# Optimization experiments

Measured on AMD Instinct MI355X. Metric: run time of the kernel, lower is better.

## Reference

```python
import jax, jax.numpy as jnp
import numpy as np

NUM_SHAPES, NUM_COLORS, NUM_CLASSES = 8, 8, 10
HID = 64
N_NODES, N_EDGES, N_REL, N_GRAPHS = 100000, 1600000, 3, 1024


def setup_inputs() -> dict:
    key = jax.random.key(0)
    ks = jax.random.split(key, 16)
    f = jnp.float32
    inp = {
        "x_idx": jax.random.randint(ks[0], (N_NODES, 2), 0, NUM_SHAPES),
        "edge_index": jax.random.randint(ks[1], (2, N_EDGES), 0, N_NODES),
        "edge_type": jax.random.randint(ks[2], (N_EDGES,), 0, N_REL),
        "batch": jnp.sort(jax.random.randint(ks[3], (N_NODES,), 0, N_GRAPHS)),
        # parameters (Linear weights stored as [in, out])
        "shape_emb": jax.random.normal(ks[4], (NUM_SHAPES, 8), f),
        "color_emb": jax.random.normal(ks[5], (NUM_COLORS, 8), f),
        "lin0_w": jax.random.normal(ks[6], (16, HID), f) * 0.1,
        "lin0_b": jnp.zeros((HID,), f),
        "r1_wrel": jax.random.normal(ks[7], (N_REL, HID, HID), f) * 0.05,
        "r1_wroot": jax.random.normal(ks[8], (HID, HID), f) * 0.05,
        "r1_b": jnp.zeros((HID,), f),
        "r2_wrel": jax.random.normal(ks[9], (N_REL, HID, HID), f) * 0.05,
        "r2_wroot": jax.random.normal(ks[10], (HID, HID), f) * 0.05,
        "r2_b": jnp.zeros((HID,), f),
        "cls_w": jax.random.normal(ks[11], (HID, NUM_CLASSES), f) * 0.1,
        "cls_b": jnp.zeros((NUM_CLASSES,), f),
    }
    return inp


def _rgcn(x, edge_index, edge_type, w_rel, w_root, b):
    # PyG RGCNConv with aggr='mean': per-relation mean of transformed neighbors + root + bias
    n = x.shape[0]
    xw = jnp.einsum('nd,rde->rne', x, w_rel)            # [R, N, H] (cheap dense)
    src, dst = edge_index[0], edge_index[1]
    msg = xw[edge_type, src]                            # [E, H] gather
    seg = edge_type * n + dst                           # combined (relation, node) segment id
    sums = jax.ops.segment_sum(msg, seg, num_segments=N_REL * n)
    cnt = jax.ops.segment_sum(jnp.ones_like(seg, dtype=x.dtype), seg, num_segments=N_REL * n)
    mean = sums / jnp.maximum(cnt, 1.0)[:, None]
    agg = mean.reshape(N_REL, n, -1).sum(axis=0)        # sum over relations
    return agg + x @ w_root + b


def reference(x_idx, edge_index, edge_type, batch,
              shape_emb, color_emb, lin0_w, lin0_b,
              r1_wrel, r1_wroot, r1_b, r2_wrel, r2_wroot, r2_b,
              cls_w, cls_b):
    x = jnp.concatenate([shape_emb[x_idx[:, 0]], color_emb[x_idx[:, 1]]], axis=1)  # [N, 16]
    x = jax.nn.relu(x @ lin0_w + lin0_b)
    x = jax.nn.relu(_rgcn(x, edge_index, edge_type, r1_wrel, r1_wroot, r1_b))
    x = jax.nn.relu(_rgcn(x, edge_index, edge_type, r2_wrel, r2_wroot, r2_b))
    # global mean pool over graphs
    sums = jax.ops.segment_sum(x, batch, num_segments=N_GRAPHS)
    cnt = jax.ops.segment_sum(jnp.ones((x.shape[0],), x.dtype), batch, num_segments=N_GRAPHS)
    pooled = sums / jnp.maximum(cnt, 1.0)[:, None]
    return pooled @ cls_w + cls_b
```

## Files before the change

### kernel.cpp

```cpp
#include <hip/hip_runtime.h>

#define NN 100000
#define NE 1600000
#define NRL 3
#define NG 1024
#define NBUCK 782
#define NXCD 8
#define PSTRIDE 384
#define BSLOTS (NXCD * PSTRIDE)
#define NKEY 384
#define OSTRIDE 392

typedef __attribute__((ext_vector_type(8))) short bf16x8;
typedef __attribute__((ext_vector_type(4))) float f32x4;

__device__ __forceinline__ int xcd_id() {
    unsigned int x;
    asm volatile("s_getreg_b32 %0, hwreg(HW_REG_XCC_ID)" : "=s"(x));
    return (int)(x & 7);
}

__device__ __forceinline__ unsigned short f2bf(float f) {
    unsigned u = __float_as_uint(f);
    unsigned r = (u + 0x7fffu + ((u >> 16) & 1u)) >> 16;
    return (unsigned short)r;
}

__global__ void k_embed(const int* __restrict__ x_idx,
                        const float* __restrict__ semb, const float* __restrict__ cemb,
                        const float* __restrict__ w, const float* __restrict__ b,
                        float* __restrict__ xout, unsigned short* __restrict__ xbf) {
    __shared__ float s_w[16 * 64];
    __shared__ float s_se[64], s_ce[64], s_b[64];
    int t = threadIdx.x;
    for (int i = t; i < 16 * 64; i += 256) s_w[i] = w[i];
    if (t < 64) { s_se[t] = semb[t]; s_ce[t] = cemb[t]; s_b[t] = b[t]; }
    __syncthreads();
    int gid = blockIdx.x * 256 + t;
    int v = gid >> 6, h = gid & 63;
    int si = x_idx[2 * v], ci = x_idx[2 * v + 1];
    float acc = s_b[h];
#pragma unroll
    for (int d = 0; d < 8; ++d) acc += s_se[si * 8 + d] * s_w[d * 64 + h];
#pragma unroll
    for (int d = 0; d < 8; ++d) acc += s_ce[ci * 8 + d] * s_w[(8 + d) * 64 + h];
    float r = fmaxf(acc, 0.f);
    xout[gid] = r;
    xbf[gid] = f2bf(r);
}

__global__ void k_bucket(const int* __restrict__ ei, const int* __restrict__ et,
                         int* __restrict__ bcnt, unsigned int* __restrict__ arena) {
    int e = blockIdx.x * 256 + threadIdx.x;
    if (e >= NE) return;
    int p = xcd_id();
    int src = __builtin_nontemporal_load(ei + e);
    int dst = __builtin_nontemporal_load(ei + NE + e);
    int rel = __builtin_nontemporal_load(et + e);
    int b = dst >> 7;
    unsigned int rec = (unsigned int)src | ((unsigned int)rel << 17) |
                       ((unsigned int)(dst & 127) << 19);
    int cell = b * NXCD + p;
    int pos = atomicAdd(&bcnt[cell], 1);
    if (pos < PSTRIDE) arena[(size_t)cell * PSTRIDE + pos] = rec;
}

__global__ __launch_bounds__(256) void k_sortbucket(
        const int* __restrict__ bcnt, unsigned int* __restrict__ arena,
        unsigned short* __restrict__ off16) {
    __shared__ unsigned int s_rec[BSLOTS];
    __shared__ unsigned int s_srt[BSLOTS];
    __shared__ int s_hist[NKEY + 1], s_start[NKEY + 1], s_pos[NKEY];
    int t = threadIdx.x;
    int b = blockIdx.x;

    for (int i = t; i < NKEY + 1; i += 256) s_hist[i] = 0;
    __syncthreads();

    int tot = 0;
#pragma unroll
    for (int p = 0; p < NXCD; ++p) {
        int c = bcnt[b * NXCD + p]; if (c > PSTRIDE) c = PSTRIDE;
        const unsigned int* src = arena + ((size_t)(b * NXCD + p)) * PSTRIDE;
        for (int i = t; i < c; i += 256) {
            unsigned int r = __builtin_nontemporal_load(src + i);
            s_rec[tot + i] = r;
            int key = ((r >> 19) & 127) * 3 + ((r >> 17) & 3);
            atomicAdd(&s_hist[key], 1);
        }
        tot += c;
    }
    __syncthreads();
    if (t == 0) {
        int run = 0;
#pragma unroll 8
        for (int k = 0; k < NKEY; ++k) { s_start[k] = run; run += s_hist[k]; }
        s_start[NKEY] = run;
    }
    __syncthreads();
    for (int i = t; i < NKEY; i += 256) s_pos[i] = s_start[i];
    __syncthreads();
    for (int i = t; i < tot; i += 256) {
        unsigned int r = s_rec[i];
        int key = ((r >> 19) & 127) * 3 + ((r >> 17) & 3);
        int p = atomicAdd(&s_pos[key], 1);
        s_srt[p] = r & 0x1FFFF;
    }
    __syncthreads();
    for (int i = t; i < tot; i += 256)
        arena[(size_t)b * BSLOTS + i] = s_srt[i];
    for (int i = t; i < NKEY + 1; i += 256)
        off16[(size_t)b * OSTRIDE + i] = (unsigned short)s_start[i];
}

__global__ void k_agg(const unsigned short* __restrict__ xbf,
                      const unsigned int* __restrict__ arena,
                      const unsigned short* __restrict__ off16,
                      unsigned short* __restrict__ K) {
    int wid = (blockIdx.x * 256 + threadIdx.x) >> 6;
    int lane = threadIdx.x & 63;
    if (wid >= NN) return;
    int v = wid;
    int b = v >> 7, dlo = v & 127;
    const unsigned short* ofs = off16 + (size_t)b * OSTRIDE + dlo * 3;
    int s0 = __builtin_amdgcn_readfirstlane((int)ofs[0]);
    int s1 = __builtin_amdgcn_readfirstlane((int)ofs[1]);
    int s2 = __builtin_amdgcn_readfirstlane((int)ofs[2]);
    int s3 = __builtin_amdgcn_readfirstlane((int)ofs[3]);
    const unsigned int* base = arena + (size_t)b * BSLOTS;

    int half = lane >> 5, sl = lane & 31;
    float2 a0 = {0.f, 0.f}, a1 = {0.f, 0.f}, a2 = {0.f, 0.f};

    int e = s0;
    for (; e + 8 <= s3; e += 8) {
#pragma unroll
        for (int k = 0; k < 4; ++k) {
            int ee = e + 2 * k + half;
            int idx = (int)base[ee];
            unsigned u = *reinterpret_cast<const unsigned*>(
                             xbf + (size_t)idx * 64 + 2 * sl);
            float f0 = __uint_as_float(u << 16);
            float f1 = __uint_as_float(u & 0xFFFF0000u);
            bool c0 = ee < s1;
            bool c2 = ee >= s2;
            bool c1 = !c0 && !c2;
            a0.x += c0 ? f0 : 0.f;  a0.y += c0 ? f1 : 0.f;
            a1.x += c1 ? f0 : 0.f;  a1.y += c1 ? f1 : 0.f;
            a2.x += c2 ? f0 : 0.f;  a2.y += c2 ? f1 : 0.f;
        }
    }
    for (; e < s3; e += 2) {
        int ee = e + half;
        bool ok = ee < s3;
        int idx = (int)base[ok ? ee : e];
        unsigned u = *reinterpret_cast<const unsigned*>(
                         xbf + (size_t)idx * 64 + 2 * sl);
        float f0 = __uint_as_float(u << 16);
        float f1 = __uint_as_float(u & 0xFFFF0000u);
        bool c0 = ok && (ee < s1);
        bool c2 = ok && (ee >= s2);
        bool c1 = ok && !(ee < s1) && (ee < s2);
        a0.x += c0 ? f0 : 0.f;  a0.y += c0 ? f1 : 0.f;
        a1.x += c1 ? f0 : 0.f;  a1.y += c1 ? f1 : 0.f;
        a2.x += c2 ? f0 : 0.f;  a2.y += c2 ? f1 : 0.f;
    }

    a0.x += __shfl_xor(a0.x, 32);  a0.y += __shfl_xor(a0.y, 32);
    a1.x += __shfl_xor(a1.x, 32);  a1.y += __shfl_xor(a1.y, 32);
    a2.x += __shfl_xor(a2.x, 32);  a2.y += __shfl_xor(a2.y, 32);

    unsigned short* Kv = K + (size_t)v * 256;
    if (lane < 32) {
        float d0 = fmaxf((float)(s1 - s0), 1.f);
        float d1 = fmaxf((float)(s2 - s1), 1.f);
        float d2 = fmaxf((float)(s3 - s2), 1.f);
        unsigned p0 = (unsigned)f2bf(a0.x / d0) | ((unsigned)f2bf(a0.y / d0) << 16);
        unsigned p1 = (unsigned)f2bf(a1.x / d1) | ((unsigned)f2bf(a1.y / d1) << 16);
        unsigned p2 = (unsigned)f2bf(a2.x / d2) | ((unsigned)f2bf(a2.y / d2) << 16);
        unsigned* Kw = reinterpret_cast<unsigned*>(Kv);
        Kw[sl]      = p0;
        Kw[32 + sl] = p1;
        Kw[64 + sl] = p2;
    }
    Kv[192 + lane] = xbf[(size_t)v * 64 + lane];
}

__global__ __launch_bounds__(512, 4) void k_transform(
        const unsigned short* __restrict__ K, const float* __restrict__ wrel,
        const float* __restrict__ wroot, const float* __restrict__ b,
        float* __restrict__ xout, unsigned short* __restrict__ xbf) {
    __shared__ __align__(16) unsigned short s_bf[4][8][64][8];
    __shared__ float s_b[64];
    int t = threadIdx.x;
    for (int i = t; i < 4 * 8 * 64 * 8; i += 512) {
        int j  = i & 7;
        int l  = (i >> 3) & 63;
        int c  = (i >> 9) & 7;
        int nt = (i >> 12) & 3;
        int k  = c * 32 + (l >> 4) * 8 + j;
        int n  = nt * 16 + (l & 15);
        const float* src = (k < 192) ? (wrel + k * 64 + n) : (wroot + (k - 192) * 64 + n);
        s_bf[nt][c][l][j] = f2bf(*src);
    }
    if (t < 64) s_b[t] = b[t];
    __syncthreads();

    int wave = t >> 6, lane = t & 63;
    int strip = blockIdx.x * 8 + wave;
    if (strip > NN / 16 - 1) strip = NN / 16 - 1;
    int v0 = strip * 16;

    const unsigned short* Ka = K + (size_t)(v0 + (lane & 15)) * 256 + (lane >> 4) * 8;

    f32x4 acc0 = {0.f, 0.f, 0.f, 0.f};
    f32x4 acc1 = {0.f, 0.f, 0.f, 0.f};
    f32x4 acc2 = {0.f, 0.f, 0.f, 0.f};
    f32x4 acc3 = {0.f, 0.f, 0.f, 0.f};

#pragma unroll
    for (int c = 0; c < 8; ++c) {
        bf16x8 a = *reinterpret_cast<const bf16x8*>(Ka + c * 32);
        bf16x8 b0 = *reinterpret_cast<const bf16x8*>(&s_bf[0][c][lane][0]);
        bf16x8 b1 = *reinterpret_cast<const bf16x8*>(&s_bf[1][c][lane][0]);
        bf16x8 b2 = *reinterpret_cast<const bf16x8*>(&s_bf[2][c][lane][0]);
        bf16x8 b3 = *reinterpret_cast<const bf16x8*>(&s_bf[3][c][lane][0]);
        acc0 = __builtin_amdgcn_mfma_f32_16x16x32_bf16(a, b0, acc0, 0, 0, 0);
        acc1 = __builtin_amdgcn_mfma_f32_16x16x32_bf16(a, b1, acc1, 0, 0, 0);
        acc2 = __builtin_amdgcn_mfma_f32_16x16x32_bf16(a, b2, acc2, 0, 0, 0);
        acc3 = __builtin_amdgcn_mfma_f32_16x16x32_bf16(a, b3, acc3, 0, 0, 0);
    }

    int col = lane & 15, rg = (lane >> 4) * 4;
#pragma unroll
    for (int r = 0; r < 4; ++r) {
        float o0 = fmaxf(acc0[r] + s_b[0  + col], 0.f);
        float o1 = fmaxf(acc1[r] + s_b[16 + col], 0.f);
        float o2 = fmaxf(acc2[r] + s_b[32 + col], 0.f);
        float o3 = fmaxf(acc3[r] + s_b[48 + col], 0.f);
        float* op = xout + (size_t)(v0 + rg + r) * 64;
        op[0  + col] = o0;
        op[16 + col] = o1;
        op[32 + col] = o2;
        op[48 + col] = o3;
        if (xbf) {
            unsigned short* ob = xbf + (size_t)(v0 + rg + r) * 64;
            ob[0  + col] = f2bf(o0);
            ob[16 + col] = f2bf(o1);
            ob[32 + col] = f2bf(o2);
            ob[48 + col] = f2bf(o3);
        }
    }
}

#define POOL_CHUNK 32
__global__ void k_pool(const float* __restrict__ x, const int* __restrict__ batch,
                       float* __restrict__ psum, int* __restrict__ pcnt) {
    int gwid = (blockIdx.x * 256 + threadIdx.x) >> 6;
    int lane = threadIdx.x & 63;
    int v0 = gwid * POOL_CHUNK;
    if (v0 >= NN) return;
    int v1 = v0 + POOL_CHUNK; if (v1 > NN) v1 = NN;
    float acc = 0.f;
    int cnt = 0;
    int gcur = batch[v0];
    for (int v = v0; v < v1; ++v) {
        int g = batch[v];
        if (g != gcur) {
            atomicAdd(&psum[gcur * 64 + lane], acc);
            if (lane == 0) atomicAdd(&pcnt[gcur], cnt);
            acc = 0.f; cnt = 0; gcur = g;
        }
        acc += x[(size_t)v * 64 + lane];
        ++cnt;
    }
    atomicAdd(&psum[gcur * 64 + lane], acc);
    if (lane == 0) atomicAdd(&pcnt[gcur], cnt);
}

__global__ void k_cls(const float* __restrict__ psum, const int* __restrict__ pcnt,
                      const float* __restrict__ w, const float* __restrict__ b,
                      float* __restrict__ out) {
    int gid = blockIdx.x * 256 + threadIdx.x;
    if (gid >= NG * 10) return;
    int g = gid / 10, c = gid % 10;
    float inv = 1.f / fmaxf((float)pcnt[g], 1.f);
    float acc = 0.f;
#pragma unroll
    for (int d = 0; d < 64; ++d) acc += psum[g * 64 + d] * w[d * 10 + c];
    out[gid] = acc * inv + b[c];
}

extern "C" void kernel_launch(void* const* d_in, const int* in_sizes, int n_in,
                              void* d_out, int out_size, void* d_ws, size_t ws_size,
                              hipStream_t stream) {
    const int*   x_idx  = (const int*)d_in[0];
    const int*   ei     = (const int*)d_in[1];
    const int*   et     = (const int*)d_in[2];
    const int*   batch  = (const int*)d_in[3];
    const float* semb   = (const float*)d_in[4];
    const float* cemb   = (const float*)d_in[5];
    const float* lin0w  = (const float*)d_in[6];
    const float* lin0b  = (const float*)d_in[7];
    const float* r1wrel = (const float*)d_in[8];
    const float* r1wroot= (const float*)d_in[9];
    const float* r1b    = (const float*)d_in[10];
    const float* r2wrel = (const float*)d_in[11];
    const float* r2wroot= (const float*)d_in[12];
    const float* r2b    = (const float*)d_in[13];
    const float* clsw   = (const float*)d_in[14];
    const float* clsb   = (const float*)d_in[15];
    float* out = (float*)d_out;

    char* ws = (char*)d_ws;
    size_t o = 0;
    auto alloc = [&](size_t bytes) -> void* {
        void* p = ws + o;
        o += (bytes + 255) & ~(size_t)255;
        return p;
    };
    int*            bcnt  = (int*)           alloc((size_t)NBUCK * NXCD * 4);
    unsigned int*   arena = (unsigned int*)  alloc((size_t)NBUCK * BSLOTS * 4);
    unsigned short* off16 = (unsigned short*)alloc((size_t)NBUCK * OSTRIDE * 2);
    float*          xA    = (float*)         alloc((size_t)NN * 64 * 4);
    float*          xB    = (float*)         alloc((size_t)NN * 64 * 4);
    unsigned short* xbf   = (unsigned short*)alloc((size_t)NN * 64 * 2);
    unsigned short* Kbuf  = (unsigned short*)alloc((size_t)NN * 256 * 2);
    float*          psum  = (float*)         alloc((size_t)NG * 64 * 4);
    int*            pcnt  = (int*)           alloc((size_t)NG * 4);

    hipMemsetAsync(bcnt, 0, (size_t)NBUCK * NXCD * 4, stream);
    hipMemsetAsync(psum, 0, (size_t)NG * 64 * 4, stream);
    hipMemsetAsync(pcnt, 0, (size_t)NG * 4, stream);

    k_embed<<<NN * 64 / 256, 256, 0, stream>>>(x_idx, semb, cemb, lin0w, lin0b, xA, xbf);

    k_bucket<<<NE / 256, 256, 0, stream>>>(ei, et, bcnt, arena);
    k_sortbucket<<<NBUCK, 256, 0, stream>>>(bcnt, arena, off16);

    k_agg<<<NN / 4, 256, 0, stream>>>(xbf, arena, off16, Kbuf);
    k_transform<<<(NN / 16 + 7) / 8, 512, 0, stream>>>(Kbuf, r1wrel, r1wroot, r1b, xB, xbf);
    k_agg<<<NN / 4, 256, 0, stream>>>(xbf, arena, off16, Kbuf);
    k_transform<<<(NN / 16 + 7) / 8, 512, 0, stream>>>(Kbuf, r2wrel, r2wroot, r2b, xA,
                                                       (unsigned short*)nullptr);

    {
        int nwaves = (NN + POOL_CHUNK - 1) / POOL_CHUNK;
        int nblk = (nwaves * 64 + 255) / 256;
        k_pool<<<nblk, 256, 0, stream>>>(xA, batch, psum, pcnt);
    }
    k_cls<<<(NG * 10 + 255) / 256, 256, 0, stream>>>(psum, pcnt, clsw, clsb, out);
}
```

Baseline: 337.8 us.

## Pre-sort edges per block in LDS before scattering into bucket arena

The bucketing kernel now processes 4096 edges per block. It builds an LDS histogram by destination bucket, reserves space with one global atomic per bucket per block, and locally sorts records in shared memory. It then writes them to the arena in contiguous runs. This replaces one global atomic per edge and scattered single-word writes, at the cost of a serial 782-entry prefix scan done by one thread, a second read of the dst array, and only 391 blocks, which lowers parallelism.

```diff
diff --git a/kernel.cpp b/kernel.cpp
--- a/kernel.cpp
+++ b/kernel.cpp
@@ -10,6 +10,7 @@
 #define BSLOTS (NXCD * PSTRIDE)
 #define NKEY 384
 #define OSTRIDE 392
+#define EB 4096
 
 typedef __attribute__((ext_vector_type(8))) short bf16x8;
 typedef __attribute__((ext_vector_type(4))) float f32x4;
@@ -49,20 +50,58 @@
     xbf[gid] = f2bf(r);
 }
 
-__global__ void k_bucket(const int* __restrict__ ei, const int* __restrict__ et,
-                         int* __restrict__ bcnt, unsigned int* __restrict__ arena) {
-    int e = blockIdx.x * 256 + threadIdx.x;
-    if (e >= NE) return;
+__global__ __launch_bounds__(256) void k_bucket(
+        const int* __restrict__ ei, const int* __restrict__ et,
+        int* __restrict__ bcnt, unsigned int* __restrict__ arena) {
+    __shared__ unsigned int   s_srt[EB];
+    __shared__ unsigned short s_skey[EB];
+    __shared__ int s_hist[NBUCK], s_start[NBUCK + 1], s_base[NBUCK], s_pos[NBUCK];
+    int t = threadIdx.x;
+    int e0 = blockIdx.x * EB;
+    int n = NE - e0; if (n > EB) n = EB;
     int p = xcd_id();
-    int src = __builtin_nontemporal_load(ei + e);
-    int dst = __builtin_nontemporal_load(ei + NE + e);
-    int rel = __builtin_nontemporal_load(et + e);
-    int b = dst >> 7;
-    unsigned int rec = (unsigned int)src | ((unsigned int)rel << 17) |
-                       ((unsigned int)(dst & 127) << 19);
-    int cell = b * NXCD + p;
-    int pos = atomicAdd(&bcnt[cell], 1);
-    if (pos < PSTRIDE) arena[(size_t)cell * PSTRIDE + pos] = rec;
+
+    for (int i = t; i < NBUCK; i += 256) s_hist[i] = 0;
+    __syncthreads();
+
+    for (int i = t; i < n; i += 256) {
+        int dst = __builtin_nontemporal_load(ei + NE + e0 + i);
+        atomicAdd(&s_hist[dst >> 7], 1);
+    }
+    __syncthreads();
+    if (t == 0) {
+        int run = 0;
+#pragma unroll 8
+        for (int k = 0; k < NBUCK; ++k) { s_start[k] = run; run += s_hist[k]; }
+        s_start[NBUCK] = run;
+    }
+    __syncthreads();
+    for (int k = t; k < NBUCK; k += 256) {
+        s_pos[k] = s_start[k];
+        s_base[k] = (s_hist[k] > 0) ? atomicAdd(&bcnt[k * NXCD + p], s_hist[k]) : 0;
+    }
+    __syncthreads();
+
+    for (int i = t; i < n; i += 256) {
+        int e = e0 + i;
+        int src = __builtin_nontemporal_load(ei + e);
+        int dst = __builtin_nontemporal_load(ei + NE + e);
+        int rel = __builtin_nontemporal_load(et + e);
+        int key = dst >> 7;
+        unsigned int rec = (unsigned int)src | ((unsigned int)rel << 17) |
+                           ((unsigned int)(dst & 127) << 19);
+        int q = atomicAdd(&s_pos[key], 1);
+        s_srt[q] = rec;
+        s_skey[q] = (unsigned short)key;
+    }
+    __syncthreads();
+
+    for (int i = t; i < n; i += 256) {
+        int key = (int)s_skey[i];
+        int off = s_base[key] + (i - s_start[key]);
+        if (off < PSTRIDE)
+            arena[((size_t)key * NXCD + p) * PSTRIDE + off] = s_srt[i];
+    }
 }
 
 __global__ __launch_bounds__(256) void k_sortbucket(
@@ -335,7 +374,7 @@
 
     k_embed<<<NN * 64 / 256, 256, 0, stream>>>(x_idx, semb, cemb, lin0w, lin0b, xA, xbf);
 
-    k_bucket<<<NE / 256, 256, 0, stream>>>(ei, et, bcnt, arena);
+    k_bucket<<<(NE + EB - 1) / EB, 256, 0, stream>>>(ei, et, bcnt, arena);
     k_sortbucket<<<NBUCK, 256, 0, stream>>>(bcnt, arena, off16);
 
     k_agg<<<NN / 4, 256, 0, stream>>>(xbf, arena, off16, Kbuf);
```

Result: faster. 298.8 us (-11.5%).
